# Optimization experiments

Hardware: AMD Instinct MI355X
Metric: run time of the kernel (lower is better)

## Reference

```python
import jax, jax.numpy as jnp
import numpy as np

N = 50000          # num nodes
E = 800000         # num edges
NUM_CLASSES = 40
FEAT_DIM = 256
FEAT_HID = 64
DEG_HID = 32
HID = 128
IN_CH = NUM_CLASSES + FEAT_HID + DEG_HID  # 136
MAX_DEG = 256      # degree-embedding table size (clip; random graph max deg << 256)


def _init_linear(key, fan_in, fan_out):
    kw, kb = jax.random.split(key)
    s = 1.0 / np.sqrt(fan_in)
    W = jax.random.uniform(kw, (fan_in, fan_out), jnp.float32, -s, s)
    b = jax.random.uniform(kb, (fan_out,), jnp.float32, -s, s)
    return W, b


def setup_inputs() -> dict:
    key = jax.random.key(0)
    ks = jax.random.split(key, 8)
    logits = jax.random.normal(ks[0], (N, NUM_CLASSES), jnp.float32)
    features = jax.random.normal(ks[1], (N, FEAT_DIM), jnp.float32)
    edge_index = jax.random.randint(ks[2], (2, E), 0, N, jnp.int32)
    Wf, bf = _init_linear(ks[3], FEAT_DIM, FEAT_HID)
    deg_table = jax.random.normal(ks[4], (MAX_DEG, DEG_HID), jnp.float32)
    W1, b1 = _init_linear(ks[5], IN_CH, HID)
    W2, b2 = _init_linear(ks[6], HID, HID)
    W3, b3 = _init_linear(ks[7], HID, NUM_CLASSES)
    return {"logits": logits, "features": features, "edge_index": edge_index,
            "Wf": Wf, "bf": bf, "deg_table": deg_table,
            "W1": W1, "b1": b1, "W2": W2, "b2": b2, "W3": W3, "b3": b3}


def reference(logits, features, edge_index, Wf, bf, deg_table, W1, b1, W2, b2, W3, b3):
    src, dst = edge_index[0], edge_index[1]
    # degree embedding: deg = degree(src) + degree(dst) on original edges
    ones_e = jnp.ones(src.shape[0], logits.dtype)
    deg = jax.ops.segment_sum(ones_e, src, num_segments=N) + \
          jax.ops.segment_sum(ones_e, dst, num_segments=N)
    deg_idx = jnp.clip(deg.astype(jnp.int32), 0, MAX_DEG - 1)
    deg_emb = deg_table[deg_idx]                              # [N, DEG_HID]

    x = jnp.concatenate([logits, features @ Wf + bf, deg_emb], axis=-1)  # [N, 136]

    # GCN normalization with self-loops (PyG gcn_norm): deg from dst column
    loop = jnp.arange(N, dtype=src.dtype)
    s = jnp.concatenate([src, loop])
    d = jnp.concatenate([dst, loop])
    dg = jax.ops.segment_sum(jnp.ones(d.shape[0], x.dtype), d, num_segments=N)
    dinv = jnp.where(dg > 0, jax.lax.rsqrt(dg), 0.0)
    norm = dinv[s] * dinv[d]                                  # [E+N]

    def conv(h, W, b):
        h = h @ W                                             # linear first
        msg = h[s] * norm[:, None]                            # gather + scale
        return jax.ops.segment_sum(msg, d, num_segments=N) + b

    x = jax.nn.relu(conv(x, W1, b1))   # dropout identity (inference)
    x = jax.nn.relu(conv(x, W2, b2))
    return conv(x, W3, b3)             # [N, NUM_CLASSES]
```

## Files before the change

### kernel.cpp

```cpp
#include <hip/hip_runtime.h>
#include <hip/hip_bf16.h>

constexpr int cN = 50000;
constexpr int cE = 800000;
constexpr int cNUM_CLASSES = 40;
constexpr int cFEAT_DIM = 256;
constexpr int cFEAT_HID = 64;
constexpr int cDEG_HID = 32;
constexpr int cHID = 128;
constexpr int cIN_CH = cNUM_CLASSES + cFEAT_HID + cDEG_HID;
constexpr int cKPAD = 160;
constexpr int cMAX_DEG = 256;

constexpr int cNCHUNK = 128;
constexpr int cCHUNK  = cE / cNCHUNK;
constexpr int cWORDS  = cN / 2;
constexpr int cHWORDS = cWORDS / 2;
constexpr int cSCANB  = (cWORDS + 255) / 256;

typedef unsigned short ushort8_t __attribute__((ext_vector_type(8)));
typedef short short8_t __attribute__((ext_vector_type(8)));
typedef float float4_t __attribute__((ext_vector_type(4)));

__device__ __forceinline__ unsigned short f2bf(float f) {
    unsigned u = __builtin_bit_cast(unsigned, f);
    u += 0x7fff + ((u >> 16) & 1);
    return (unsigned short)(u >> 16);
}
__device__ __forceinline__ float bf2f(unsigned short s) {
    unsigned u = ((unsigned)s) << 16;
    return __builtin_bit_cast(float, u);
}

__global__ __launch_bounds__(256) void prep_kernel(const int* __restrict__ edge,
                                                   unsigned* __restrict__ partial,
                                                   const float* __restrict__ Wf,
                                                   const float* __restrict__ W1,
                                                   const float* __restrict__ W2,
                                                   const float* __restrict__ W3,
                                                   unsigned short* __restrict__ Wtf,
                                                   unsigned short* __restrict__ Wt1,
                                                   unsigned short* __restrict__ Wt2,
                                                   unsigned short* __restrict__ Wt3) {
    __shared__ unsigned lds[cHWORDS];
    const int b = blockIdx.x, tid = threadIdx.x;
    if (b < 512) {
        const int cb = b & (cNCHUNK - 1);
        const int half = (b >> 7) & 1;
        const int which = b >> 8;
        for (int i = tid; i < cHWORDS; i += 256) lds[i] = 0;
        __syncthreads();
        const int* ids = edge + (size_t)which * cE + (size_t)cb * cCHUNK;
        const int lo = half * (cN / 2), hi = lo + cN / 2;
        const int wbase = half * cHWORDS;
        for (int i = tid; i < cCHUNK; i += 256) {
            int v = ids[i];
            if (v >= lo && v < hi)
                atomicAdd(&lds[(v >> 1) - wbase], 1u << ((v & 1) * 16));
        }
        __syncthreads();
        unsigned* outp = partial + ((size_t)which * cNCHUNK + cb) * cWORDS + wbase;
        for (int i = tid; i < cHWORDS; i += 256) outp[i] = lds[i];
        return;
    }
    int i = (b - 512) * 256 + tid;
    if (i < 16384) {
        int n = i >> 8, k = i & 255;
        Wtf[i] = f2bf(Wf[k * cFEAT_HID + n]);
        return;
    }
    i -= 16384;
    if (i < 128 * cKPAD) {
        int n = i / cKPAD, k = i - n * cKPAD;
        Wt1[i] = (k < cIN_CH) ? f2bf(W1[k * cHID + n]) : 0;
        return;
    }
    i -= 128 * cKPAD;
    if (i < 128 * 128) {
        int n = i >> 7, k = i & 127;
        Wt2[i] = f2bf(W2[k * cHID + n]);
        return;
    }
    i -= 128 * 128;
    if (i < 48 * 128) {
        int n = i >> 7, k = i & 127;
        Wt3[i] = (n < cNUM_CLASSES) ? f2bf(W3[k * cNUM_CLASSES + n]) : 0;
    }
}

__global__ __launch_bounds__(256) void mega_scan_kernel(unsigned* __restrict__ partial,
                                                        int* __restrict__ count_src,
                                                        int* __restrict__ count_dst,
                                                        int* __restrict__ rowptr,
                                                        float* __restrict__ dinv,
                                                        int* __restrict__ desc) {
    const int b = blockIdx.x, tid = threadIdx.x;
    const int w = b * 256 + tid;
    unsigned slo = 0, shi = 0, plo = 0, phi = 0;
    if (w < cWORDS) {
        const unsigned* ps = partial + w;
        for (int c = 0; c < cNCHUNK; ++c) {
            unsigned v = ps[(size_t)c * cWORDS];
            slo += v & 0xFFFFu; shi += v >> 16;
        }
        *(int2*)&count_src[2 * w] = make_int2((int)slo, (int)shi);
        unsigned* pd = partial + (size_t)cNCHUNK * cWORDS + w;
        for (int c = 0; c < cNCHUNK; ++c) {
            unsigned v = pd[(size_t)c * cWORDS];
            pd[(size_t)c * cWORDS] = plo | (phi << 16);
            plo += v & 0xFFFFu; phi += v >> 16;
        }
        *(int2*)&count_dst[2 * w] = make_int2((int)plo, (int)phi);
    }
    __shared__ int s[256];
    __shared__ int pre[cSCANB];
    int tot = (int)(plo + phi);
    s[tid] = tot;
    __syncthreads();
    #pragma unroll
    for (int off = 1; off < 256; off <<= 1) {
        int t = (tid >= off) ? s[tid - off] : 0;
        __syncthreads();
        s[tid] += t;
        __syncthreads();
    }
    int ex_local = s[tid] - tot;
    int block_total = s[255];
    if (tid == 0) atomicExch(&desc[b], block_total + 1);
    if (tid < b) {
        int v;
        do { v = atomicAdd(&desc[tid], 0); } while (v == 0);
        s[tid] = v - 1;
    }
    __syncthreads();
    if (tid >= b) s[tid] = 0;
    __syncthreads();
    #pragma unroll
    for (int off = 128; off > 0; off >>= 1) {
        if (tid < off) s[tid] += s[tid + off];
        __syncthreads();
    }
    int base = s[0] + ex_local;
    if (w < cWORDS) {
        rowptr[2 * w]     = base;
        rowptr[2 * w + 1] = base + (int)plo;
        dinv[2 * w]     = rsqrtf((float)(plo + 1));
        dinv[2 * w + 1] = rsqrtf((float)(phi + 1));
    }
    if (b == 0 && tid == 0) rowptr[cN] = cE;
    (void)pre;
}

__global__ __launch_bounds__(256) void scatter2_kernel(const int* __restrict__ edge,
                                                       const unsigned* __restrict__ partial,
                                                       const int* __restrict__ rowptr,
                                                       int* __restrict__ adj) {
    __shared__ unsigned lds[cHWORDS];
    const int b = blockIdx.x, tid = threadIdx.x;
    const int cb = b & (cNCHUNK - 1);
    const int half = b >> 7;
    const int wbase = half * cHWORDS;
    const unsigned* pp = partial + ((size_t)cNCHUNK + cb) * cWORDS + wbase;
    for (int i = tid; i < cHWORDS; i += 256) lds[i] = pp[i];
    __syncthreads();
    const int* srcs = edge + (size_t)cb * cCHUNK;
    const int* dsts = edge + cE + (size_t)cb * cCHUNK;
    const int lo = half * (cN / 2), hi = lo + cN / 2;
    for (int i = tid; i < cCHUNK; i += 256) {
        int d = dsts[i];
        if (d >= lo && d < hi) {
            int sh = (d & 1) * 16;
            unsigned old = atomicAdd(&lds[(d >> 1) - wbase], 1u << sh);
            int off = (int)((old >> sh) & 0xFFFFu);
            adj[rowptr[d] + off] = srcs[i];
        }
    }
}

__global__ __launch_bounds__(256) void frontend_kernel(const float* __restrict__ logits,
                                                       const int* __restrict__ count_src,
                                                       const int* __restrict__ count_dst,
                                                       const float* __restrict__ deg_table,
                                                       unsigned short* __restrict__ xb) {
    constexpr int W = cNUM_CLASSES + cDEG_HID + 24;
    int idx = blockIdx.x * 256 + threadIdx.x;
    if (idx >= cN * W) return;
    int i = idx / W;
    int j = idx - i * W;
    if (j < cNUM_CLASSES) {
        xb[(size_t)i * cKPAD + j] = f2bf(logits[(size_t)i * cNUM_CLASSES + j]);
    } else {
        int jj = j - cNUM_CLASSES;
        unsigned short v = 0;
        if (jj < cDEG_HID) {
            int deg = count_src[i] + count_dst[i];
            if (deg > cMAX_DEG - 1) deg = cMAX_DEG - 1;
            v = f2bf(deg_table[deg * cDEG_HID + jj]);
        }
        xb[(size_t)i * cKPAD + cNUM_CLASSES + cFEAT_HID + jj] = v;
    }
}

template <int ASTR, int KTOT, int NT, int OSTR, int OOFF, int OUTC, bool AFP32, bool BIAS>
__global__ __launch_bounds__(256) void mfma_gemm(const void* __restrict__ Av,
                                                 const unsigned short* __restrict__ Bt,
                                                 const float* __restrict__ bias,
                                                 unsigned short* __restrict__ out) {
    __shared__ unsigned short As[64 * 32];
    __shared__ unsigned short Bs[NT * 16 * 32];

    const int tid = threadIdx.x;
    const int wave = tid >> 6;
    const int lane = tid & 63;
    const int m15 = lane & 15;
    const int q = lane >> 4;
    const int rowbase = blockIdx.x * 64;

    float4_t acc[NT];
    #pragma unroll
    for (int t = 0; t < NT; ++t) acc[t] = (float4_t){0.f, 0.f, 0.f, 0.f};

    const int arow = tid >> 2;
    const int akq = (tid & 3) * 8;
    int gr = rowbase + arow;
    if (gr > cN - 1) gr = cN - 1;

    for (int k0 = 0; k0 < KTOT; k0 += 32) {
        if constexpr (AFP32) {
            const float* ap = (const float*)Av + (size_t)gr * ASTR + k0 + akq;
            float4 v0 = *(const float4*)ap;
            float4 v1 = *(const float4*)(ap + 4);
            ushort8_t o = { f2bf(v0.x), f2bf(v0.y), f2bf(v0.z), f2bf(v0.w),
                            f2bf(v1.x), f2bf(v1.y), f2bf(v1.z), f2bf(v1.w) };
            *(ushort8_t*)&As[arow * 32 + akq] = o;
        } else {
            const unsigned short* ap = (const unsigned short*)Av + (size_t)gr * ASTR + k0 + akq;
            *(ushort8_t*)&As[arow * 32 + akq] = *(const ushort8_t*)ap;
        }
        for (int i = tid; i < NT * 64; i += 256) {
            int n = i >> 2;
            int kq = (i & 3) * 8;
            *(ushort8_t*)&Bs[n * 32 + kq] = *(const ushort8_t*)&Bt[(size_t)n * KTOT + k0 + kq];
        }
        __syncthreads();

        short8_t a = *(const short8_t*)&As[(wave * 16 + m15) * 32 + q * 8];
        #pragma unroll
        for (int t = 0; t < NT; ++t) {
            short8_t b = *(const short8_t*)&Bs[(t * 16 + m15) * 32 + q * 8];
            acc[t] = __builtin_amdgcn_mfma_f32_16x16x32_bf16(a, b, acc[t], 0, 0, 0);
        }
        __syncthreads();
    }

    #pragma unroll
    for (int t = 0; t < NT; ++t) {
        int col = t * 16 + m15;
        if (OUTC % 16 != 0 && col >= OUTC) continue;
        float bv = BIAS ? bias[col] : 0.f;
        #pragma unroll
        for (int r = 0; r < 4; ++r) {
            int row = rowbase + wave * 16 + q * 4 + r;
            if (row < cN)
                out[(size_t)row * OSTR + OOFF + col] = f2bf(acc[t][r] + bv);
        }
    }
}

template <bool RELU>
__global__ __launch_bounds__(128) void agg_bf128(const unsigned short* __restrict__ t,
                                                 const int* __restrict__ rowptr,
                                                 const int* __restrict__ adj,
                                                 const float* __restrict__ dinv,
                                                 const float* __restrict__ b,
                                                 unsigned short* __restrict__ outb) {
    const int tid = threadIdx.x;
    const int lane = tid & 15;
    const int row = blockIdx.x * 8 + (tid >> 4);
    if (row >= cN) return;
    const int c = lane * 8;
    const float di = dinv[row];
    int e = rowptr[row];
    const int end = rowptr[row + 1];
    float a0[8], a1[8];
    #pragma unroll
    for (int k = 0; k < 8; ++k) { a0[k] = 0.f; a1[k] = 0.f; }
    for (; e + 1 < end; e += 2) {
        int j0 = adj[e], j1 = adj[e + 1];
        float v0 = dinv[j0], v1 = dinv[j1];
        ushort8_t t0 = *(const ushort8_t*)&t[(size_t)j0 * cHID + c];
        ushort8_t t1 = *(const ushort8_t*)&t[(size_t)j1 * cHID + c];
        #pragma unroll
        for (int k = 0; k < 8; ++k) {
            a0[k] += v0 * bf2f(t0[k]);
            a1[k] += v1 * bf2f(t1[k]);
        }
    }
    if (e < end) {
        int j0 = adj[e];
        float v0 = dinv[j0];
        ushort8_t t0 = *(const ushort8_t*)&t[(size_t)j0 * cHID + c];
        #pragma unroll
        for (int k = 0; k < 8; ++k) a0[k] += v0 * bf2f(t0[k]);
    }
    ushort8_t ts = *(const ushort8_t*)&t[(size_t)row * cHID + c];
    const float d2 = di * di;
    ushort8_t o;
    #pragma unroll
    for (int k = 0; k < 8; ++k) {
        float r = di * (a0[k] + a1[k]) + d2 * bf2f(ts[k]) + b[c + k];
        if (RELU) r = fmaxf(r, 0.f);
        o[k] = f2bf(r);
    }
    *(ushort8_t*)&outb[(size_t)row * cHID + c] = o;
}

__global__ __launch_bounds__(128) void agg_bf40(const unsigned short* __restrict__ t,
                                                const int* __restrict__ rowptr,
                                                const int* __restrict__ adj,
                                                const float* __restrict__ dinv,
                                                const float* __restrict__ b,
                                                float* __restrict__ out) {
    const int tid = threadIdx.x;
    const int lane = tid & 7;
    const int row = blockIdx.x * 16 + (tid >> 3);
    if (row >= cN) return;
    const int c = lane * 8;
    if (c >= cNUM_CLASSES) return;
    const float di = dinv[row];
    int e = rowptr[row];
    const int end = rowptr[row + 1];
    float a0[8], a1[8];
    #pragma unroll
    for (int k = 0; k < 8; ++k) { a0[k] = 0.f; a1[k] = 0.f; }
    for (; e + 1 < end; e += 2) {
        int j0 = adj[e], j1 = adj[e + 1];
        float v0 = dinv[j0], v1 = dinv[j1];
        ushort8_t t0 = *(const ushort8_t*)&t[(size_t)j0 * cNUM_CLASSES + c];
        ushort8_t t1 = *(const ushort8_t*)&t[(size_t)j1 * cNUM_CLASSES + c];
        #pragma unroll
        for (int k = 0; k < 8; ++k) {
            a0[k] += v0 * bf2f(t0[k]);
            a1[k] += v1 * bf2f(t1[k]);
        }
    }
    if (e < end) {
        int j0 = adj[e];
        float v0 = dinv[j0];
        ushort8_t t0 = *(const ushort8_t*)&t[(size_t)j0 * cNUM_CLASSES + c];
        #pragma unroll
        for (int k = 0; k < 8; ++k) a0[k] += v0 * bf2f(t0[k]);
    }
    ushort8_t ts = *(const ushort8_t*)&t[(size_t)row * cNUM_CLASSES + c];
    const float d2 = di * di;
    float r[8];
    #pragma unroll
    for (int k = 0; k < 8; ++k) r[k] = di * (a0[k] + a1[k]) + d2 * bf2f(ts[k]) + b[c + k];
    float4 v0 = make_float4(r[0], r[1], r[2], r[3]);
    float4 v1 = make_float4(r[4], r[5], r[6], r[7]);
    *(float4*)&out[(size_t)row * cNUM_CLASSES + c] = v0;
    *(float4*)&out[(size_t)row * cNUM_CLASSES + c + 4] = v1;
}

extern "C" void kernel_launch(void* const* d_in, const int* in_sizes, int n_in,
                              void* d_out, int out_size, void* d_ws, size_t ws_size,
                              hipStream_t stream) {
    const float* logits    = (const float*)d_in[0];
    const float* features  = (const float*)d_in[1];
    const int*   edge      = (const int*)d_in[2];
    const float* Wf        = (const float*)d_in[3];
    const float* bf        = (const float*)d_in[4];
    const float* deg_table = (const float*)d_in[5];
    const float* W1        = (const float*)d_in[6];
    const float* b1        = (const float*)d_in[7];
    const float* W2        = (const float*)d_in[8];
    const float* b2        = (const float*)d_in[9];
    const float* W3        = (const float*)d_in[10];
    const float* b3        = (const float*)d_in[11];
    float* out = (float*)d_out;

    int* count_src = (int*)d_ws;
    int* count_dst = count_src + cN;
    int* rowptr    = count_dst + cN;
    int* adj       = rowptr + cN + 16;
    int* desc      = adj + cE;
    float* dinv    = (float*)(desc + 128);
    unsigned short* xb  = (unsigned short*)(dinv + cN);
    unsigned short* tb  = xb + (size_t)cN * cKPAD;
    unsigned short* hb  = tb + (size_t)cN * cHID;
    unsigned short* Wtf = hb + (size_t)cN * cHID;
    unsigned short* Wt1 = Wtf + 64 * 256;
    unsigned short* Wt2 = Wt1 + 128 * cKPAD;
    unsigned short* Wt3 = Wt2 + 128 * 128;
    unsigned* partial = (unsigned*)(Wt3 + 48 * 128);

    hipMemsetAsync(desc, 0, 128 * sizeof(int), stream);

    constexpr int WTOT = 16384 + 128 * cKPAD + 128 * 128 + 48 * 128;
    constexpr int WBLK = (WTOT + 255) / 256;
    prep_kernel<<<512 + WBLK, 256, 0, stream>>>(edge, partial, Wf, W1, W2, W3, Wtf, Wt1, Wt2, Wt3);

    mega_scan_kernel<<<cSCANB, 256, 0, stream>>>(partial, count_src, count_dst, rowptr, dinv, desc);

    scatter2_kernel<<<256, 256, 0, stream>>>(edge, partial, rowptr, adj);

    frontend_kernel<<<(cN * 96 + 255) / 256, 256, 0, stream>>>(logits, count_src, count_dst, deg_table, xb);

    constexpr int MB = (cN + 63) / 64;

    mfma_gemm<cFEAT_DIM, 256, 4, cKPAD, cNUM_CLASSES, 64, true, true>
        <<<MB, 256, 0, stream>>>(features, Wtf, bf, xb);

    mfma_gemm<cKPAD, cKPAD, 8, cHID, 0, cHID, false, false>
        <<<MB, 256, 0, stream>>>(xb, Wt1, nullptr, tb);
    agg_bf128<true><<<(cN + 7) / 8, 128, 0, stream>>>(tb, rowptr, adj, dinv, b1, hb);

    mfma_gemm<cHID, cHID, 8, cHID, 0, cHID, false, false>
        <<<MB, 256, 0, stream>>>(hb, Wt2, nullptr, tb);
    agg_bf128<true><<<(cN + 7) / 8, 128, 0, stream>>>(tb, rowptr, adj, dinv, b2, hb);

    mfma_gemm<cHID, cHID, 3, cNUM_CLASSES, 0, cNUM_CLASSES, false, false>
        <<<MB, 256, 0, stream>>>(hb, Wt3, nullptr, tb);
    agg_bf40<<<(cN + 15) / 16, 128, 0, stream>>>(tb, rowptr, adj, dinv, b3, out);
}
```

Baseline: 322.9 us.

## Split each row's neighbor aggregation across four lane groups per wave

The aggregation kernels now give each destination row a full 64-lane wave, with four 16-lane groups each handling every fourth edge. Partial sums are combined with cross-lane shuffles. This puts more gather loads in flight per row and evens out load across rows of different degree. The cost is shuffle reductions and a quarter of the threads per wave. The 40-class kernel switches to 4-wide loads, and some lanes in each group sit idle.

Result: slower. 341.2 us (+5.6%).

```diff
diff --git a/kernel.cpp b/kernel.cpp
--- a/kernel.cpp
+++ b/kernel.cpp
@@ -19,6 +19,7 @@
 constexpr int cSCANB  = (cWORDS + 255) / 256;
 
 typedef unsigned short ushort8_t __attribute__((ext_vector_type(8)));
+typedef unsigned short ushort4_t __attribute__((ext_vector_type(4)));
 typedef short short8_t __attribute__((ext_vector_type(8)));
 typedef float float4_t __attribute__((ext_vector_type(4)));
 
@@ -113,7 +114,6 @@
         *(int2*)&count_dst[2 * w] = make_int2((int)plo, (int)phi);
     }
     __shared__ int s[256];
-    __shared__ int pre[cSCANB];
     int tot = (int)(plo + phi);
     s[tid] = tot;
     __syncthreads();
@@ -148,7 +148,6 @@
         dinv[2 * w + 1] = rsqrtf((float)(phi + 1));
     }
     if (b == 0 && tid == 0) rowptr[cN] = cE;
-    (void)pre;
 }
 
 __global__ __launch_bounds__(256) void scatter2_kernel(const int* __restrict__ edge,
@@ -268,98 +267,102 @@
 }
 
 template <bool RELU>
-__global__ __launch_bounds__(128) void agg_bf128(const unsigned short* __restrict__ t,
-                                                 const int* __restrict__ rowptr,
-                                                 const int* __restrict__ adj,
-                                                 const float* __restrict__ dinv,
-                                                 const float* __restrict__ b,
-                                                 unsigned short* __restrict__ outb) {
-    const int tid = threadIdx.x;
-    const int lane = tid & 15;
-    const int row = blockIdx.x * 8 + (tid >> 4);
-    if (row >= cN) return;
-    const int c = lane * 8;
-    const float di = dinv[row];
-    int e = rowptr[row];
-    const int end = rowptr[row + 1];
-    float a0[8], a1[8];
-    #pragma unroll
-    for (int k = 0; k < 8; ++k) { a0[k] = 0.f; a1[k] = 0.f; }
-    for (; e + 1 < end; e += 2) {
-        int j0 = adj[e], j1 = adj[e + 1];
-        float v0 = dinv[j0], v1 = dinv[j1];
-        ushort8_t t0 = *(const ushort8_t*)&t[(size_t)j0 * cHID + c];
-        ushort8_t t1 = *(const ushort8_t*)&t[(size_t)j1 * cHID + c];
-        #pragma unroll
-        for (int k = 0; k < 8; ++k) {
-            a0[k] += v0 * bf2f(t0[k]);
-            a1[k] += v1 * bf2f(t1[k]);
-        }
-    }
-    if (e < end) {
-        int j0 = adj[e];
-        float v0 = dinv[j0];
-        ushort8_t t0 = *(const ushort8_t*)&t[(size_t)j0 * cHID + c];
-        #pragma unroll
-        for (int k = 0; k < 8; ++k) a0[k] += v0 * bf2f(t0[k]);
-    }
-    ushort8_t ts = *(const ushort8_t*)&t[(size_t)row * cHID + c];
-    const float d2 = di * di;
-    ushort8_t o;
-    #pragma unroll
-    for (int k = 0; k < 8; ++k) {
-        float r = di * (a0[k] + a1[k]) + d2 * bf2f(ts[k]) + b[c + k];
-        if (RELU) r = fmaxf(r, 0.f);
-        o[k] = f2bf(r);
-    }
-    *(ushort8_t*)&outb[(size_t)row * cHID + c] = o;
-}
-
-__global__ __launch_bounds__(128) void agg_bf40(const unsigned short* __restrict__ t,
+__global__ __launch_bounds__(256) void agg_g128(const unsigned short* __restrict__ t,
                                                 const int* __restrict__ rowptr,
                                                 const int* __restrict__ adj,
                                                 const float* __restrict__ dinv,
                                                 const float* __restrict__ b,
-                                                float* __restrict__ out) {
+                                                unsigned short* __restrict__ outb) {
     const int tid = threadIdx.x;
-    const int lane = tid & 7;
-    const int row = blockIdx.x * 16 + (tid >> 3);
+    const int wave = tid >> 6;
+    const int lane = tid & 63;
+    const int g = lane >> 4;
+    const int l = lane & 15;
+    const int row = blockIdx.x * 4 + wave;
     if (row >= cN) return;
-    const int c = lane * 8;
-    if (c >= cNUM_CLASSES) return;
+    const int c = l * 8;
     const float di = dinv[row];
-    int e = rowptr[row];
-    const int end = rowptr[row + 1];
-    float a0[8], a1[8];
-    #pragma unroll
-    for (int k = 0; k < 8; ++k) { a0[k] = 0.f; a1[k] = 0.f; }
-    for (; e + 1 < end; e += 2) {
-        int j0 = adj[e], j1 = adj[e + 1];
-        float v0 = dinv[j0], v1 = dinv[j1];
-        ushort8_t t0 = *(const ushort8_t*)&t[(size_t)j0 * cNUM_CLASSES + c];
-        ushort8_t t1 = *(const ushort8_t*)&t[(size_t)j1 * cNUM_CLASSES + c];
+    const int beg = rowptr[row], end = rowptr[row + 1];
+    float acc[8];
+    #pragma unroll
+    for (int k = 0; k < 8; ++k) acc[k] = 0.f;
+    for (int e = beg; e < end; e += 4) {
+        int ee = e + g;
+        bool valid = ee < end;
+        int j = valid ? adj[ee] : row;
+        float v = valid ? dinv[j] : 0.f;
+        ushort8_t tv = *(const ushort8_t*)&t[(size_t)j * cHID + c];
+        #pragma unroll
+        for (int k = 0; k < 8; ++k) acc[k] += v * bf2f(tv[k]);
+    }
+    #pragma unroll
+    for (int k = 0; k < 8; ++k) {
+        float a = acc[k];
+        a += __shfl_xor(a, 16, 64);
+        a += __shfl_xor(a, 32, 64);
+        acc[k] = a;
+    }
+    if (g == 0) {
+        ushort8_t ts = *(const ushort8_t*)&t[(size_t)row * cHID + c];
+        const float d2 = di * di;
+        ushort8_t o;
         #pragma unroll
         for (int k = 0; k < 8; ++k) {
-            a0[k] += v0 * bf2f(t0[k]);
-            a1[k] += v1 * bf2f(t1[k]);
-        }
-    }
-    if (e < end) {
-        int j0 = adj[e];
-        float v0 = dinv[j0];
-        ushort8_t t0 = *(const ushort8_t*)&t[(size_t)j0 * cNUM_CLASSES + c];
+            float r = di * acc[k] + d2 * bf2f(ts[k]) + b[c + k];
+            if (RELU) r = fmaxf(r, 0.f);
+            o[k] = f2bf(r);
+        }
+        *(ushort8_t*)&outb[(size_t)row * cHID + c] = o;
+    }
+}
+
+__global__ __launch_bounds__(256) void agg_g40(const unsigned short* __restrict__ t,
+                                               const int* __restrict__ rowptr,
+                                               const int* __restrict__ adj,
+                                               const float* __restrict__ dinv,
+                                               const float* __restrict__ b,
+                                               float* __restrict__ out) {
+    const int tid = threadIdx.x;
+    const int wave = tid >> 6;
+    const int lane = tid & 63;
+    const int g = lane >> 4;
+    const int l = lane & 15;
+    const int row = blockIdx.x * 4 + wave;
+    if (row >= cN) return;
+    const int c = l * 4;
+    const bool act = c < cNUM_CLASSES;
+    const float di = dinv[row];
+    const int beg = rowptr[row], end = rowptr[row + 1];
+    float acc[4];
+    #pragma unroll
+    for (int k = 0; k < 4; ++k) acc[k] = 0.f;
+    for (int e = beg; e < end; e += 4) {
+        int ee = e + g;
+        bool valid = (ee < end) && act;
+        int j = (ee < end) ? adj[ee] : row;
+        float v = valid ? dinv[j] : 0.f;
+        int cc = act ? c : 0;
+        ushort4_t tv = *(const ushort4_t*)&t[(size_t)j * cNUM_CLASSES + cc];
         #pragma unroll
-        for (int k = 0; k < 8; ++k) a0[k] += v0 * bf2f(t0[k]);
-    }
-    ushort8_t ts = *(const ushort8_t*)&t[(size_t)row * cNUM_CLASSES + c];
-    const float d2 = di * di;
-    float r[8];
-    #pragma unroll
-    for (int k = 0; k < 8; ++k) r[k] = di * (a0[k] + a1[k]) + d2 * bf2f(ts[k]) + b[c + k];
-    float4 v0 = make_float4(r[0], r[1], r[2], r[3]);
-    float4 v1 = make_float4(r[4], r[5], r[6], r[7]);
-    *(float4*)&out[(size_t)row * cNUM_CLASSES + c] = v0;
-    *(float4*)&out[(size_t)row * cNUM_CLASSES + c + 4] = v1;
+        for (int k = 0; k < 4; ++k) acc[k] += v * bf2f(tv[k]);
+    }
+    #pragma unroll
+    for (int k = 0; k < 4; ++k) {
+        float a = acc[k];
+        a += __shfl_xor(a, 16, 64);
+        a += __shfl_xor(a, 32, 64);
+        acc[k] = a;
+    }
+    if (g == 0 && act) {
+        ushort4_t ts = *(const ushort4_t*)&t[(size_t)row * cNUM_CLASSES + c];
+        const float d2 = di * di;
+        float4 r;
+        r.x = di * acc[0] + d2 * bf2f(ts[0]) + b[c];
+        r.y = di * acc[1] + d2 * bf2f(ts[1]) + b[c + 1];
+        r.z = di * acc[2] + d2 * bf2f(ts[2]) + b[c + 2];
+        r.w = di * acc[3] + d2 * bf2f(ts[3]) + b[c + 3];
+        *(float4*)&out[(size_t)row * cNUM_CLASSES + c] = r;
+    }
 }
 
 extern "C" void kernel_launch(void* const* d_in, const int* in_sizes, int n_in,
@@ -413,13 +416,13 @@
 
     mfma_gemm<cKPAD, cKPAD, 8, cHID, 0, cHID, false, false>
         <<<MB, 256, 0, stream>>>(xb, Wt1, nullptr, tb);
-    agg_bf128<true><<<(cN + 7) / 8, 128, 0, stream>>>(tb, rowptr, adj, dinv, b1, hb);
+    agg_g128<true><<<(cN + 3) / 4, 256, 0, stream>>>(tb, rowptr, adj, dinv, b1, hb);
 
     mfma_gemm<cHID, cHID, 8, cHID, 0, cHID, false, false>
         <<<MB, 256, 0, stream>>>(hb, Wt2, nullptr, tb);
-    agg_bf128<true><<<(cN + 7) / 8, 128, 0, stream>>>(tb, rowptr, adj, dinv, b2, hb);
+    agg_g128<true><<<(cN + 3) / 4, 256, 0, stream>>>(tb, rowptr, adj, dinv, b2, hb);
 
     mfma_gemm<cHID, cHID, 3, cNUM_CLASSES, 0, cNUM_CLASSES, false, false>
         <<<MB, 256, 0, stream>>>(hb, Wt3, nullptr, tb);
-    agg_bf40<<<(cN + 15) / 16, 128, 0, stream>>>(tb, rowptr, adj, dinv, b3, out);
-}
+    agg_g40<<<(cN + 3) / 4, 256, 0, stream>>>(tb, rowptr, adj, dinv, b3, out);
+}
```

## Fold feature projection into first GCN weight and fuse front-end into GEMM

Applied to the files above, without the earlier changes.

Precomputes Wf·W1 (and bf·W1 as a bias) so the feature linear layer and the first conv linear become a single GEMM over a 352-wide concatenated input. The new fused GEMM reads logits, raw features and the degree-embedding row directly and converts them to bf16 on the fly, which removes the frontend kernel, the feature GEMM and the intermediate xb buffer. The scan kernel now writes clipped degree indices instead of separate src and dst counts. The trade-off is a larger K per row (352 instead of 160), a small matrix product added to the prep kernel, and scalar per-element LDS stores for the A tile.

Result: faster. 293.5 us (-9.1%).

```diff
diff --git a/kernel.cpp b/kernel.cpp
--- a/kernel.cpp
+++ b/kernel.cpp
@@ -8,9 +8,8 @@
 constexpr int cFEAT_HID = 64;
 constexpr int cDEG_HID = 32;
 constexpr int cHID = 128;
-constexpr int cIN_CH = cNUM_CLASSES + cFEAT_HID + cDEG_HID;
-constexpr int cKPAD = 160;
 constexpr int cMAX_DEG = 256;
+constexpr int cKF = 352;
 
 constexpr int cNCHUNK = 128;
 constexpr int cCHUNK  = cE / cNCHUNK;
@@ -35,13 +34,14 @@
 __global__ __launch_bounds__(256) void prep_kernel(const int* __restrict__ edge,
                                                    unsigned* __restrict__ partial,
                                                    const float* __restrict__ Wf,
+                                                   const float* __restrict__ bfv,
                                                    const float* __restrict__ W1,
                                                    const float* __restrict__ W2,
                                                    const float* __restrict__ W3,
-                                                   unsigned short* __restrict__ Wtf,
-                                                   unsigned short* __restrict__ Wt1,
+                                                   unsigned short* __restrict__ Btc,
                                                    unsigned short* __restrict__ Wt2,
-                                                   unsigned short* __restrict__ Wt3) {
+                                                   unsigned short* __restrict__ Wt3,
+                                                   float* __restrict__ bias2) {
     __shared__ unsigned lds[cHWORDS];
     const int b = blockIdx.x, tid = threadIdx.x;
     if (b < 512) {
@@ -63,36 +63,54 @@
         for (int i = tid; i < cHWORDS; i += 256) outp[i] = lds[i];
         return;
     }
-    int i = (b - 512) * 256 + tid;
-    if (i < 16384) {
-        int n = i >> 8, k = i & 255;
-        Wtf[i] = f2bf(Wf[k * cFEAT_HID + n]);
+    if (b < 648) {
+        int i = (b - 512) * 256 + tid;
+        if (i < 12288) {
+            int n = i / 96, r = i - (i / 96) * 96;
+            unsigned short v;
+            if (r < 40)       v = f2bf(W1[r * cHID + n]);
+            else if (r < 72)  v = f2bf(W1[(104 + r - 40) * cHID + n]);
+            else              v = 0;
+            int k = (r < 40) ? r : (r < 72 ? 296 + (r - 40) : 328 + (r - 72));
+            Btc[n * cKF + k] = v;
+            return;
+        }
+        i -= 12288;
+        if (i < 16384) {
+            int n = i >> 7, k = i & 127;
+            Wt2[n * cHID + k] = f2bf(W2[k * cHID + n]);
+            return;
+        }
+        i -= 16384;
+        if (i < 6144) {
+            int n = i >> 7, k = i & 127;
+            Wt3[n * cHID + k] = (n < cNUM_CLASSES) ? f2bf(W3[k * cNUM_CLASSES + n]) : 0;
+        }
         return;
     }
-    i -= 16384;
-    if (i < 128 * cKPAD) {
-        int n = i / cKPAD, k = i - n * cKPAD;
-        Wt1[i] = (k < cIN_CH) ? f2bf(W1[k * cHID + n]) : 0;
+    if (b < 776) {
+        int i = (b - 648) * 256 + tid;
+        int kf = i >> 7, n = i & 127;
+        float s = 0.f;
+        #pragma unroll 8
+        for (int j = 0; j < cFEAT_HID; ++j)
+            s += Wf[kf * cFEAT_HID + j] * W1[(40 + j) * cHID + n];
+        Btc[n * cKF + 40 + kf] = f2bf(s);
         return;
     }
-    i -= 128 * cKPAD;
-    if (i < 128 * 128) {
-        int n = i >> 7, k = i & 127;
-        Wt2[i] = f2bf(W2[k * cHID + n]);
-        return;
-    }
-    i -= 128 * 128;
-    if (i < 48 * 128) {
-        int n = i >> 7, k = i & 127;
-        Wt3[i] = (n < cNUM_CLASSES) ? f2bf(W3[k * cNUM_CLASSES + n]) : 0;
+    if (tid < cHID) {
+        float s = 0.f;
+        #pragma unroll 8
+        for (int j = 0; j < cFEAT_HID; ++j)
+            s += bfv[j] * W1[(40 + j) * cHID + tid];
+        bias2[tid] = s;
     }
 }
 
 __global__ __launch_bounds__(256) void mega_scan_kernel(unsigned* __restrict__ partial,
-                                                        int* __restrict__ count_src,
-                                                        int* __restrict__ count_dst,
                                                         int* __restrict__ rowptr,
                                                         float* __restrict__ dinv,
+                                                        int* __restrict__ degidx,
                                                         int* __restrict__ desc) {
     const int b = blockIdx.x, tid = threadIdx.x;
     const int w = b * 256 + tid;
@@ -103,17 +121,17 @@
             unsigned v = ps[(size_t)c * cWORDS];
             slo += v & 0xFFFFu; shi += v >> 16;
         }
-        *(int2*)&count_src[2 * w] = make_int2((int)slo, (int)shi);
         unsigned* pd = partial + (size_t)cNCHUNK * cWORDS + w;
         for (int c = 0; c < cNCHUNK; ++c) {
             unsigned v = pd[(size_t)c * cWORDS];
             pd[(size_t)c * cWORDS] = plo | (phi << 16);
             plo += v & 0xFFFFu; phi += v >> 16;
         }
-        *(int2*)&count_dst[2 * w] = make_int2((int)plo, (int)phi);
+        int d0 = (int)(slo + plo), d1 = (int)(shi + phi);
+        degidx[2 * w]     = d0 > cMAX_DEG - 1 ? cMAX_DEG - 1 : d0;
+        degidx[2 * w + 1] = d1 > cMAX_DEG - 1 ? cMAX_DEG - 1 : d1;
     }
     __shared__ int s[256];
-    __shared__ int pre[cSCANB];
     int tot = (int)(plo + phi);
     s[tid] = tot;
     __syncthreads();
@@ -148,7 +166,6 @@
         dinv[2 * w + 1] = rsqrtf((float)(phi + 1));
     }
     if (b == 0 && tid == 0) rowptr[cN] = cE;
-    (void)pre;
 }
 
 __global__ __launch_bounds__(256) void scatter2_kernel(const int* __restrict__ edge,
@@ -177,35 +194,14 @@
     }
 }
 
-__global__ __launch_bounds__(256) void frontend_kernel(const float* __restrict__ logits,
-                                                       const int* __restrict__ count_src,
-                                                       const int* __restrict__ count_dst,
-                                                       const float* __restrict__ deg_table,
-                                                       unsigned short* __restrict__ xb) {
-    constexpr int W = cNUM_CLASSES + cDEG_HID + 24;
-    int idx = blockIdx.x * 256 + threadIdx.x;
-    if (idx >= cN * W) return;
-    int i = idx / W;
-    int j = idx - i * W;
-    if (j < cNUM_CLASSES) {
-        xb[(size_t)i * cKPAD + j] = f2bf(logits[(size_t)i * cNUM_CLASSES + j]);
-    } else {
-        int jj = j - cNUM_CLASSES;
-        unsigned short v = 0;
-        if (jj < cDEG_HID) {
-            int deg = count_src[i] + count_dst[i];
-            if (deg > cMAX_DEG - 1) deg = cMAX_DEG - 1;
-            v = f2bf(deg_table[deg * cDEG_HID + jj]);
-        }
-        xb[(size_t)i * cKPAD + cNUM_CLASSES + cFEAT_HID + jj] = v;
-    }
-}
-
-template <int ASTR, int KTOT, int NT, int OSTR, int OOFF, int OUTC, bool AFP32, bool BIAS>
-__global__ __launch_bounds__(256) void mfma_gemm(const void* __restrict__ Av,
-                                                 const unsigned short* __restrict__ Bt,
-                                                 const float* __restrict__ bias,
-                                                 unsigned short* __restrict__ out) {
+__global__ __launch_bounds__(256) void gemm_fused(const float* __restrict__ logits,
+                                                  const float* __restrict__ features,
+                                                  const float* __restrict__ deg_table,
+                                                  const int* __restrict__ degidx,
+                                                  const unsigned short* __restrict__ Btc,
+                                                  const float* __restrict__ bias2,
+                                                  unsigned short* __restrict__ out) {
+    constexpr int NT = 8;
     __shared__ unsigned short As[64 * 32];
     __shared__ unsigned short Bs[NT * 16 * 32];
 
@@ -224,19 +220,74 @@
     const int akq = (tid & 3) * 8;
     int gr = rowbase + arow;
     if (gr > cN - 1) gr = cN - 1;
+    const int didx = degidx[gr];
+
+    for (int k0 = 0; k0 < cKF; k0 += 32) {
+        #pragma unroll
+        for (int h = 0; h < 2; ++h) {
+            int k4 = k0 + akq + h * 4;
+            float4 v = make_float4(0.f, 0.f, 0.f, 0.f);
+            if (k4 < 40)       v = *(const float4*)&logits[(size_t)gr * cNUM_CLASSES + k4];
+            else if (k4 < 296) v = *(const float4*)&features[(size_t)gr * cFEAT_DIM + (k4 - 40)];
+            else if (k4 < 328) v = *(const float4*)&deg_table[didx * cDEG_HID + (k4 - 296)];
+            unsigned short* dst = &As[arow * 32 + akq + h * 4];
+            dst[0] = f2bf(v.x); dst[1] = f2bf(v.y); dst[2] = f2bf(v.z); dst[3] = f2bf(v.w);
+        }
+        for (int i = tid; i < NT * 64; i += 256) {
+            int n = i >> 2;
+            int kq = (i & 3) * 8;
+            *(ushort8_t*)&Bs[n * 32 + kq] = *(const ushort8_t*)&Btc[(size_t)n * cKF + k0 + kq];
+        }
+        __syncthreads();
+
+        short8_t a = *(const short8_t*)&As[(wave * 16 + m15) * 32 + q * 8];
+        #pragma unroll
+        for (int t = 0; t < NT; ++t) {
+            short8_t bfr = *(const short8_t*)&Bs[(t * 16 + m15) * 32 + q * 8];
+            acc[t] = __builtin_amdgcn_mfma_f32_16x16x32_bf16(a, bfr, acc[t], 0, 0, 0);
+        }
+        __syncthreads();
+    }
+
+    #pragma unroll
+    for (int t = 0; t < NT; ++t) {
+        int col = t * 16 + m15;
+        float bv = bias2[col];
+        #pragma unroll
+        for (int r = 0; r < 4; ++r) {
+            int row = rowbase + wave * 16 + q * 4 + r;
+            if (row < cN)
+                out[(size_t)row * cHID + col] = f2bf(acc[t][r] + bv);
+        }
+    }
+}
+
+template <int KTOT, int NT, int OSTR, int OUTC>
+__global__ __launch_bounds__(256) void mfma_gemm(const unsigned short* __restrict__ A,
+                                                 const unsigned short* __restrict__ Bt,
+                                                 unsigned short* __restrict__ out) {
+    __shared__ unsigned short As[64 * 32];
+    __shared__ unsigned short Bs[NT * 16 * 32];
+
+    const int tid = threadIdx.x;
+    const int wave = tid >> 6;
+    const int lane = tid & 63;
+    const int m15 = lane & 15;
+    const int q = lane >> 4;
+    const int rowbase = blockIdx.x * 64;
+
+    float4_t acc[NT];
+    #pragma unroll
+    for (int t = 0; t < NT; ++t) acc[t] = (float4_t){0.f, 0.f, 0.f, 0.f};
+
+    const int arow = tid >> 2;
+    const int akq = (tid & 3) * 8;
+    int gr = rowbase + arow;
+    if (gr > cN - 1) gr = cN - 1;
 
     for (int k0 = 0; k0 < KTOT; k0 += 32) {
-        if constexpr (AFP32) {
-            const float* ap = (const float*)Av + (size_t)gr * ASTR + k0 + akq;
-            float4 v0 = *(const float4*)ap;
-            float4 v1 = *(const float4*)(ap + 4);
-            ushort8_t o = { f2bf(v0.x), f2bf(v0.y), f2bf(v0.z), f2bf(v0.w),
-                            f2bf(v1.x), f2bf(v1.y), f2bf(v1.z), f2bf(v1.w) };
-            *(ushort8_t*)&As[arow * 32 + akq] = o;
-        } else {
-            const unsigned short* ap = (const unsigned short*)Av + (size_t)gr * ASTR + k0 + akq;
-            *(ushort8_t*)&As[arow * 32 + akq] = *(const ushort8_t*)ap;
-        }
+        *(ushort8_t*)&As[arow * 32 + akq] =
+            *(const ushort8_t*)&A[(size_t)gr * KTOT + k0 + akq];
         for (int i = tid; i < NT * 64; i += 256) {
             int n = i >> 2;
             int kq = (i & 3) * 8;
@@ -257,12 +308,11 @@
     for (int t = 0; t < NT; ++t) {
         int col = t * 16 + m15;
         if (OUTC % 16 != 0 && col >= OUTC) continue;
-        float bv = BIAS ? bias[col] : 0.f;
         #pragma unroll
         for (int r = 0; r < 4; ++r) {
             int row = rowbase + wave * 16 + q * 4 + r;
             if (row < cN)
-                out[(size_t)row * OSTR + OOFF + col] = f2bf(acc[t][r] + bv);
+                out[(size_t)row * OSTR + col] = f2bf(acc[t][r]);
         }
     }
 }
@@ -369,7 +419,7 @@
     const float* features  = (const float*)d_in[1];
     const int*   edge      = (const int*)d_in[2];
     const float* Wf        = (const float*)d_in[3];
-    const float* bf        = (const float*)d_in[4];
+    const float* bfv       = (const float*)d_in[4];
     const float* deg_table = (const float*)d_in[5];
     const float* W1        = (const float*)d_in[6];
     const float* b1        = (const float*)d_in[7];
@@ -379,47 +429,36 @@
     const float* b3        = (const float*)d_in[11];
     float* out = (float*)d_out;
 
-    int* count_src = (int*)d_ws;
-    int* count_dst = count_src + cN;
-    int* rowptr    = count_dst + cN;
+    int* rowptr    = (int*)d_ws;
     int* adj       = rowptr + cN + 16;
     int* desc      = adj + cE;
-    float* dinv    = (float*)(desc + 128);
-    unsigned short* xb  = (unsigned short*)(dinv + cN);
-    unsigned short* tb  = xb + (size_t)cN * cKPAD;
+    int* degidx    = desc + 128;
+    float* dinv    = (float*)(degidx + cN);
+    float* bias2   = dinv + cN;
+    unsigned short* tb  = (unsigned short*)(bias2 + 128);
     unsigned short* hb  = tb + (size_t)cN * cHID;
-    unsigned short* Wtf = hb + (size_t)cN * cHID;
-    unsigned short* Wt1 = Wtf + 64 * 256;
-    unsigned short* Wt2 = Wt1 + 128 * cKPAD;
-    unsigned short* Wt3 = Wt2 + 128 * 128;
-    unsigned* partial = (unsigned*)(Wt3 + 48 * 128);
+    unsigned short* Btc = hb + (size_t)cN * cHID;
+    unsigned short* Wt2 = Btc + 128 * cKF;
+    unsigned short* Wt3 = Wt2 + 128 * cHID;
+    unsigned* partial = (unsigned*)(Wt3 + 48 * cHID);
 
     hipMemsetAsync(desc, 0, 128 * sizeof(int), stream);
 
-    constexpr int WTOT = 16384 + 128 * cKPAD + 128 * 128 + 48 * 128;
-    constexpr int WBLK = (WTOT + 255) / 256;
-    prep_kernel<<<512 + WBLK, 256, 0, stream>>>(edge, partial, Wf, W1, W2, W3, Wtf, Wt1, Wt2, Wt3);
-
-    mega_scan_kernel<<<cSCANB, 256, 0, stream>>>(partial, count_src, count_dst, rowptr, dinv, desc);
+    prep_kernel<<<777, 256, 0, stream>>>(edge, partial, Wf, bfv, W1, W2, W3,
+                                         Btc, Wt2, Wt3, bias2);
+
+    mega_scan_kernel<<<cSCANB, 256, 0, stream>>>(partial, rowptr, dinv, degidx, desc);
 
     scatter2_kernel<<<256, 256, 0, stream>>>(edge, partial, rowptr, adj);
 
-    frontend_kernel<<<(cN * 96 + 255) / 256, 256, 0, stream>>>(logits, count_src, count_dst, deg_table, xb);
-
     constexpr int MB = (cN + 63) / 64;
 
-    mfma_gemm<cFEAT_DIM, 256, 4, cKPAD, cNUM_CLASSES, 64, true, true>
-        <<<MB, 256, 0, stream>>>(features, Wtf, bf, xb);
-
-    mfma_gemm<cKPAD, cKPAD, 8, cHID, 0, cHID, false, false>
-        <<<MB, 256, 0, stream>>>(xb, Wt1, nullptr, tb);
+    gemm_fused<<<MB, 256, 0, stream>>>(logits, features, deg_table, degidx, Btc, bias2, tb);
     agg_bf128<true><<<(cN + 7) / 8, 128, 0, stream>>>(tb, rowptr, adj, dinv, b1, hb);
 
-    mfma_gemm<cHID, cHID, 8, cHID, 0, cHID, false, false>
-        <<<MB, 256, 0, stream>>>(hb, Wt2, nullptr, tb);
+    mfma_gemm<cHID, 8, cHID, cHID><<<MB, 256, 0, stream>>>(hb, Wt2, tb);
     agg_bf128<true><<<(cN + 7) / 8, 128, 0, stream>>>(tb, rowptr, adj, dinv, b2, hb);
 
-    mfma_gemm<cHID, cHID, 3, cNUM_CLASSES, 0, cNUM_CLASSES, false, false>
-        <<<MB, 256, 0, stream>>>(hb, Wt3, nullptr, tb);
+    mfma_gemm<cHID, 3, cNUM_CLASSES, cNUM_CLASSES><<<MB, 256, 0, stream>>>(hb, Wt3, tb);
     agg_bf40<<<(cN + 15) / 16, 128, 0, stream>>>(tb, rowptr, adj, dinv, b3, out);
 }
```
